# Performance work log

Hardware: AMD Instinct MI355X
Metric: run time of the kernel (lower is better)

The kernel has to match this reference:

```python
import jax, jax.numpy as jnp
import numpy as np
from jax import lax

VOCAB = 4096
HID = 1024
BATCH = 64
SEQ = 256


def setup_inputs() -> dict:
    key = jax.random.key(0)
    ks = jax.random.split(key, 8)
    s = 0.02  # small init to keep gates out of saturation
    return {
        "tokens": jax.random.randint(ks[0], (BATCH, SEQ), 0, VOCAB),
        "W1": jax.random.normal(ks[1], (4, VOCAB + HID, HID), jnp.float32) * s,
        "b1": jax.random.normal(ks[2], (4, HID), jnp.float32) * s,
        "W2": jax.random.normal(ks[3], (4, 2 * HID, HID), jnp.float32) * s,
        "b2": jax.random.normal(ks[4], (4, HID), jnp.float32) * s,
        "Wout": jax.random.normal(ks[5], (HID, VOCAB), jnp.float32) * s,
        "bout": jax.random.normal(ks[6], (VOCAB,), jnp.float32) * s,
    }


def _cell(x, H, C, W, b):
    # x: [B, in], H/C: [B, Hid]; W: [4, in+Hid, Hid] stacked f,i,o,c_tilde
    cat = jnp.concatenate([x, H], axis=1)                 # [B, in+Hid]
    g = jnp.einsum('bd,gdh->gbh', cat, W) + b[:, None, :] # [4, B, Hid]
    f = jax.nn.sigmoid(g[0])
    i = jax.nn.sigmoid(g[1])
    o = jax.nn.sigmoid(g[2])
    c_tilde = jnp.tanh(g[3])
    C = f * C + i * c_tilde
    H = o * jnp.tanh(C)
    return H, C


def reference(tokens, W1, b1, W2, b2, Wout, bout):
    B = tokens.shape[0]
    V = Wout.shape[1]
    Hn = W1.shape[2]
    z = jnp.zeros((B, Hn), dtype=Wout.dtype)
    init = (z, z, z, z)  # (H1, C1, H2, C2), zero initial states

    def step(carry, tok):
        H1, C1, H2, C2 = carry
        x = jax.nn.one_hot(tok, V, dtype=Wout.dtype)  # [B, V]
        H1, C1 = _cell(x, H1, C1, W1, b1)
        H2, C2 = _cell(H1, H2, C2, W2, b2)
        Y = H2 @ Wout + bout                          # [B, V]
        return (H1, C1, H2, C2), Y

    carry, ys = lax.scan(step, init, tokens.T)  # ys: [S, B, V]
    out = ys.reshape(-1, V)                     # torch.cat(outputs, dim=0)
    H1, C1, H2, C2 = carry
    return out, H1, C1, H2, C2
```

## Files before the change

kernel.cpp:

```cpp
#include <hip/hip_runtime.h>
#include <hip/hip_bf16.h>

typedef float f32x4 __attribute__((ext_vector_type(4)));
typedef short bf16x8 __attribute__((ext_vector_type(8)));
typedef unsigned int u32x4 __attribute__((ext_vector_type(4)));

#define MFMA16x32(a,b,c) __builtin_amdgcn_mfma_f32_16x16x32_bf16((a),(b),(c),0,0,0)

__device__ __forceinline__ unsigned short f2bf(float f) {
  unsigned u = __float_as_uint(f);
  u += 0x7fffu + ((u >> 16) & 1u);
  return (unsigned short)(u >> 16);
}

__device__ __forceinline__ void ast16(unsigned short* p, unsigned short v) {
  __hip_atomic_store(p, v, __ATOMIC_RELAXED, __HIP_MEMORY_SCOPE_AGENT);
}

__device__ __forceinline__ u32x4 ld16_bypass(const void* p) {
  u32x4 r;
  asm volatile("global_load_dwordx4 %0, %1, off sc0 sc1" : "=v"(r) : "v"(p) : "memory");
  return r;
}

#define WS_G1BLOB 0ull
#define WS_G3BLOB 8388608ull
#define WS_WOUTT  25165824ull
#define WS_H1RING 33554432ull
#define WS_SYNC   34078720ull
#define WS_H2ALL  34095104ull

#define SLSTRIDE 8

__global__ void k_init(unsigned* __restrict__ p, int n) {
  int i = blockIdx.x * blockDim.x + threadIdx.x;
  for (; i < n; i += gridDim.x * blockDim.x) p[i] = 0u;
}

__global__ void k_pack_g1(const float* __restrict__ W1, unsigned short* __restrict__ blob) {
  int gtid = blockIdx.x * 256 + threadIdx.x;
  int lane = gtid & 63, kk = (gtid >> 6) & 31, w = gtid >> 11;
  int c = lane & 15, q = lane >> 4;
  int g = c >> 2, h = w * 4 + (c & 3);
  bf16x8 s;
#pragma unroll
  for (int j = 0; j < 8; ++j) {
    int k = kk * 32 + q * 8 + j;
    float v = W1[(size_t)g * 5242880u + (size_t)(4096 + k) * 1024u + h];
    ((unsigned short*)&s)[j] = f2bf(v);
  }
  ((bf16x8*)blob)[(size_t)(w * 32 + kk) * 64 + lane] = s;
}

__global__ void k_pack_g3(const float* __restrict__ W2, unsigned short* __restrict__ blob) {
  int gtid = blockIdx.x * 256 + threadIdx.x;
  int lane = gtid & 63, kk = (gtid >> 6) & 63, w = gtid >> 12;
  int c = lane & 15, q = lane >> 4;
  int g = c >> 2, h = w * 4 + (c & 3);
  bf16x8 s;
#pragma unroll
  for (int j = 0; j < 8; ++j) {
    int klocal = (kk & 31) * 32 + q * 8 + j;
    int d = (kk < 32) ? (1024 + klocal) : klocal;
    float v = W2[(size_t)g * 2097152u + (size_t)d * 1024u + h];
    ((unsigned short*)&s)[j] = f2bf(v);
  }
  ((bf16x8*)blob)[(size_t)(w * 64 + kk) * 64 + lane] = s;
}

__global__ void k_pack_woutT(const float* __restrict__ Wout, unsigned short* __restrict__ wT) {
  int gtid = blockIdx.x * 256 + threadIdx.x;
  int k = gtid & 1023, n = gtid >> 10;
  wT[(size_t)n * 1024 + k] = f2bf(Wout[(size_t)k * 4096 + n]);
}

__device__ __forceinline__ void wait_slots(const unsigned* __restrict__ slots,
                                           unsigned epoch, unsigned* __restrict__ poison) {
  if (threadIdx.x < 64) {
    unsigned guard = 0;
    for (;;) {
      unsigned v0 = __hip_atomic_load(&slots[threadIdx.x * SLSTRIDE],
                                      __ATOMIC_RELAXED, __HIP_MEMORY_SCOPE_AGENT);
      unsigned v1 = __hip_atomic_load(&slots[(threadIdx.x + 64) * SLSTRIDE],
                                      __ATOMIC_RELAXED, __HIP_MEMORY_SCOPE_AGENT);
      unsigned v = v0 < v1 ? v0 : v1;
      if (__all((int)(v >= epoch))) break;
      __builtin_amdgcn_s_sleep(1);
      if (((++guard) & 1023u) == 0u) {
        if (guard > (1u << 18) ||
            __hip_atomic_load(poison, __ATOMIC_RELAXED, __HIP_MEMORY_SCOPE_AGENT) != 0u) {
          __hip_atomic_store(poison, 1u, __ATOMIC_RELAXED, __HIP_MEMORY_SCOPE_AGENT);
          break;
        }
      }
    }
  }
  __syncthreads();
}

__device__ __forceinline__ void publish_slot(unsigned* __restrict__ slots,
                                             int myslot, unsigned epoch) {
  asm volatile("s_waitcnt vmcnt(0)" ::: "memory");
  __syncthreads();
  if (threadIdx.x == 0) {
    __hip_atomic_store(&slots[myslot * SLSTRIDE], epoch,
                       __ATOMIC_RELAXED, __HIP_MEMORY_SCOPE_AGENT);
  }
}

__device__ __forceinline__ void stage_H(const unsigned short* __restrict__ Hsrc,
                                        unsigned short* __restrict__ Hs) {
  asm volatile("s_waitcnt vmcnt(0)" ::: "memory");
  const int tid = threadIdx.x;
  const char* base = (const char*)Hsrc;
  const int rowlo = tid >> 7;
  const int x = (tid & 127) * 16;
  u32x4 v[4][8];
#define ISSUE_BATCH(B) \
  _Pragma("unroll") \
  for (int r8 = 0; r8 < 8; ++r8) { \
    int row = ((B) * 8 + r8) * 2 + rowlo; \
    v[B][r8] = ld16_bypass(base + row * 2048 + (x ^ ((row & 7) << 4))); \
  }
#define WRITE_BATCH(B) \
  _Pragma("unroll") \
  for (int r8 = 0; r8 < 8; ++r8) \
    *(u32x4*)((char*)Hs + ((B) * 8 + r8) * 4096 + tid * 16) = v[B][r8];

  ISSUE_BATCH(0)
  ISSUE_BATCH(1)
  asm volatile("s_waitcnt vmcnt(8)" ::: "memory");
  __builtin_amdgcn_sched_barrier(0);
  WRITE_BATCH(0)
  ISSUE_BATCH(2)
  asm volatile("s_waitcnt vmcnt(8)" ::: "memory");
  __builtin_amdgcn_sched_barrier(0);
  WRITE_BATCH(1)
  ISSUE_BATCH(3)
  asm volatile("s_waitcnt vmcnt(8)" ::: "memory");
  __builtin_amdgcn_sched_barrier(0);
  WRITE_BATCH(2)
  asm volatile("s_waitcnt vmcnt(0)" ::: "memory");
  __builtin_amdgcn_sched_barrier(0);
  WRITE_BATCH(3)
#undef ISSUE_BATCH
#undef WRITE_BATCH
}

__device__ __forceinline__ bf16x8 lds_frag(const unsigned short* __restrict__ Hs,
                                           int row, int colb) {
  return *(const bf16x8*)((const char*)Hs + row * 2048 + (colb ^ ((row & 7) << 4)));
}

__global__ __launch_bounds__(256, 1) void k_lstm(
    const int* __restrict__ tokens, const float* __restrict__ W1,
    const float* __restrict__ b1, const float* __restrict__ b2,
    const unsigned short* __restrict__ g1blob, const unsigned short* __restrict__ g3blob,
    unsigned short* __restrict__ h1ring, unsigned short* __restrict__ h2all,
    float* __restrict__ outF, unsigned* __restrict__ syncbase)
{
  __shared__ unsigned short Hs[65536];
  __shared__ float red[2][64][16];

  const int tid = threadIdx.x, lane = tid & 63, widx = tid >> 6, bid = blockIdx.x;
  const int c = lane & 15, q = lane >> 4;
  const bool isG1 = bid < 128;
  const int myslot = isG1 ? bid : bid - 128;
  const int ct = widx >> 1, kh = widx & 1;
  const int w = myslot * 2 + ct;
  const int g = c >> 2;
  const int hcol = w * 4 + (c & 3);
  const int h_ew = w * 4 + (lane & 3);

  unsigned* g1slots = syncbase;
  unsigned* g3slots = syncbase + 1024;
  unsigned* poison  = syncbase + 2048;

  bf16x8 Breg[32];
  {
    const bf16x8* blob1 = (const bf16x8*)g1blob;
    const bf16x8* blob3 = (const bf16x8*)g3blob;
    if (isG1) {
#pragma unroll
      for (int j = 0; j < 16; ++j)
        Breg[j] = blob1[(size_t)(w * 32 + kh * 16 + j) * 64 + lane];
    } else {
#pragma unroll
      for (int j = 0; j < 16; ++j) {
        Breg[j]      = blob3[(size_t)(w * 64 + kh * 16 + j) * 64 + lane];
        Breg[16 + j] = blob3[(size_t)(w * 64 + 32 + kh * 16 + j) * 64 + lane];
      }
    }
  }
  const float biasv = isG1 ? b1[g * 1024 + hcol] : b2[g * 1024 + hcol];

  float Cst[16];
#pragma unroll
  for (int i = 0; i < 16; ++i) Cst[i] = 0.f;

  float gv[16];
  if (isG1 && kh == 0) {
#pragma unroll
    for (int m = 0; m < 4; ++m)
#pragma unroll
      for (int r = 0; r < 4; ++r) {
        int b_ = m * 16 + q * 4 + r;
        int tk = tokens[b_ * 256];
        gv[m * 4 + r] = W1[(size_t)g * 5242880u + (size_t)tk * 1024u + hcol];
      }
  }

  f32x4 acc[4];

  if (isG1) {
#pragma clang loop unroll(disable)
    for (int t = 0; t < 256; ++t) {
      if (t > 0) wait_slots(g1slots, (unsigned)t, poison);

      int tk2[16];
      if (kh == 0) {
        const int tn = (t < 255) ? t + 1 : 255;
#pragma unroll
        for (int m = 0; m < 4; ++m)
#pragma unroll
          for (int r = 0; r < 4; ++r)
            tk2[m * 4 + r] = tokens[(m * 16 + q * 4 + r) * 256 + tn];
      }

#pragma unroll
      for (int m = 0; m < 4; ++m) acc[m] = (f32x4){0.f, 0.f, 0.f, 0.f};
      if (t > 0) {
        stage_H(h1ring + ((t - 1) & 3) * 65536, Hs);
        __syncthreads();
#pragma unroll
        for (int j = 0; j < 16; ++j) {
#pragma unroll
          for (int m = 0; m < 4; ++m) {
            bf16x8 a = lds_frag(Hs, m * 16 + c, (kh * 16 + j) * 64 + q * 16);
            acc[m] = MFMA16x32(a, Breg[j], acc[m]);
          }
        }
      }
      if (t >= 4) wait_slots(g3slots, (unsigned)(t - 3), poison);
      else __syncthreads();

      if (kh == 1) {
#pragma unroll
        for (int m = 0; m < 4; ++m) *(f32x4*)&red[ct][lane][m * 4] = acc[m];
      }
      __syncthreads();
      if (kh == 0) {
#pragma unroll
        for (int m = 0; m < 4; ++m) acc[m] += *(const f32x4*)&red[ct][lane][m * 4];
#pragma unroll
        for (int m = 0; m < 4; ++m) {
#pragma unroll
          for (int r = 0; r < 4; ++r) {
            float v = acc[m][r] + gv[m * 4 + r] + biasv;
            const int sb = (lane & 48) | (lane & 3);
            float vf = __shfl(v, sb, 64);
            float vi = __shfl(v, sb | 4, 64);
            float vo = __shfl(v, sb | 8, 64);
            float vc = __shfl(v, sb | 12, 64);
            float fg = 1.f / (1.f + __expf(-vf));
            float ig = 1.f / (1.f + __expf(-vi));
            float og = 1.f / (1.f + __expf(-vo));
            float e2 = __expf(2.f * vc);
            float ct_ = (e2 - 1.f) / (e2 + 1.f);
            float Cn = fg * Cst[m * 4 + r] + ig * ct_;
            Cst[m * 4 + r] = Cn;
            float e2c = __expf(2.f * Cn);
            float Hn = og * (e2c - 1.f) / (e2c + 1.f);
            if ((lane & 12) == 0) {
              int row = m * 16 + q * 4 + r;
              ast16(&h1ring[(t & 3) * 65536 + row * 1024 + h_ew], f2bf(Hn));
              if (t == 255) {
                outF[row * 1024 + h_ew] = Hn;
                outF[65536 + row * 1024 + h_ew] = Cn;
              }
            }
          }
        }
      }
      publish_slot(g1slots, myslot, (unsigned)(t + 1));

      if (kh == 0) {
#pragma unroll
        for (int i = 0; i < 16; ++i)
          gv[i] = W1[(size_t)g * 5242880u + (size_t)tk2[i] * 1024u + hcol];
      }
    }
  } else {
#pragma clang loop unroll(disable)
    for (int t = 0; t < 256; ++t) {
      wait_slots(g1slots, (unsigned)(t + 1), poison);
#pragma unroll
      for (int m = 0; m < 4; ++m)
        acc[m] = (kh == 0) ? (f32x4){biasv, biasv, biasv, biasv}
                           : (f32x4){0.f, 0.f, 0.f, 0.f};
      stage_H(h1ring + (t & 3) * 65536, Hs);
      __syncthreads();
#pragma unroll
      for (int j = 0; j < 16; ++j) {
#pragma unroll
        for (int m = 0; m < 4; ++m) {
          bf16x8 a = lds_frag(Hs, m * 16 + c, (kh * 16 + j) * 64 + q * 16);
          acc[m] = MFMA16x32(a, Breg[16 + j], acc[m]);
        }
      }

      if (t > 0) {
        wait_slots(g3slots, (unsigned)t, poison);
        stage_H(h2all + (size_t)(t - 1) * 65536, Hs);
        __syncthreads();
#pragma unroll
        for (int j = 0; j < 16; ++j) {
#pragma unroll
          for (int m = 0; m < 4; ++m) {
            bf16x8 a = lds_frag(Hs, m * 16 + c, (kh * 16 + j) * 64 + q * 16);
            acc[m] = MFMA16x32(a, Breg[j], acc[m]);
          }
        }
      }

      if (kh == 1) {
#pragma unroll
        for (int m = 0; m < 4; ++m) *(f32x4*)&red[ct][lane][m * 4] = acc[m];
      }
      __syncthreads();
      if (kh == 0) {
#pragma unroll
        for (int m = 0; m < 4; ++m) acc[m] += *(const f32x4*)&red[ct][lane][m * 4];
#pragma unroll
        for (int m = 0; m < 4; ++m) {
#pragma unroll
          for (int r = 0; r < 4; ++r) {
            float v = acc[m][r];
            const int sb = (lane & 48) | (lane & 3);
            float vf = __shfl(v, sb, 64);
            float vi = __shfl(v, sb | 4, 64);
            float vo = __shfl(v, sb | 8, 64);
            float vc = __shfl(v, sb | 12, 64);
            float fg = 1.f / (1.f + __expf(-vf));
            float ig = 1.f / (1.f + __expf(-vi));
            float og = 1.f / (1.f + __expf(-vo));
            float e2 = __expf(2.f * vc);
            float ct_ = (e2 - 1.f) / (e2 + 1.f);
            float Cn = fg * Cst[m * 4 + r] + ig * ct_;
            Cst[m * 4 + r] = Cn;
            float e2c = __expf(2.f * Cn);
            float Hn = og * (e2c - 1.f) / (e2c + 1.f);
            if ((lane & 12) == 0) {
              int row = m * 16 + q * 4 + r;
              ast16(&h2all[((size_t)t * 64 + row) * 1024 + h_ew], f2bf(Hn));
              if (t == 255) {
                outF[131072 + row * 1024 + h_ew] = Hn;
                outF[196608 + row * 1024 + h_ew] = Cn;
              }
            }
          }
        }
      }
      publish_slot(g3slots, myslot, (unsigned)(t + 1));
    }
  }
}

__global__ __launch_bounds__(256, 2) void k_gemm_out(
    const unsigned short* __restrict__ A, const unsigned short* __restrict__ Bt,
    const float* __restrict__ bout, float* __restrict__ C)
{
  __shared__ unsigned short As[128 * 32];
  __shared__ unsigned short Bs[128 * 32];
  const int tid = threadIdx.x, lane = tid & 63, wv = tid >> 6;
  const int c = lane & 15, q = lane >> 4;
  const int bn = blockIdx.x & 31, bm = blockIdx.x >> 5;
  const int wm = wv >> 1, wn = wv & 1;

  f32x4 acc[4][4];
#pragma unroll
  for (int m = 0; m < 4; ++m)
#pragma unroll
    for (int n = 0; n < 4; ++n) acc[m][n] = (f32x4){0.f, 0.f, 0.f, 0.f};

  const unsigned short* Abase = A + (size_t)(bm * 128) * 1024;
  const unsigned short* Bbase = Bt + (size_t)(bn * 128) * 1024;

  for (int kt = 0; kt < 32; ++kt) {
    if (kt) __syncthreads();
#pragma unroll
    for (int ch = 0; ch < 2; ++ch) {
      int o = ch * 4096 + tid * 16;
      int row = o >> 6;
      int ks = (o & 63) >> 1;
      *(bf16x8*)&As[o >> 1] = *(const bf16x8*)(Abase + (size_t)row * 1024 + kt * 32 + ks);
      *(bf16x8*)&Bs[o >> 1] = *(const bf16x8*)(Bbase + (size_t)row * 1024 + kt * 32 + ks);
    }
    __syncthreads();
    bf16x8 af[4], bfr[4];
#pragma unroll
    for (int m = 0; m < 4; ++m) af[m] = *(const bf16x8*)&As[(wm * 64 + m * 16 + c) * 32 + q * 8];
#pragma unroll
    for (int n = 0; n < 4; ++n) bfr[n] = *(const bf16x8*)&Bs[(wn * 64 + n * 16 + c) * 32 + q * 8];
#pragma unroll
    for (int m = 0; m < 4; ++m)
#pragma unroll
      for (int n = 0; n < 4; ++n) acc[m][n] = MFMA16x32(af[m], bfr[n], acc[m][n]);
  }

#pragma unroll
  for (int n = 0; n < 4; ++n) {
    int col = bn * 128 + wn * 64 + n * 16 + c;
    float bo = bout[col];
#pragma unroll
    for (int m = 0; m < 4; ++m) {
      int row0 = bm * 128 + wm * 64 + m * 16 + q * 4;
#pragma unroll
      for (int r = 0; r < 4; ++r)
        C[(size_t)(row0 + r) * 4096 + col] = acc[m][n][r] + bo;
    }
  }
}

extern "C" void kernel_launch(void* const* d_in, const int* in_sizes, int n_in,
                              void* d_out, int out_size, void* d_ws, size_t ws_size,
                              hipStream_t stream) {
  const int* tokens = (const int*)d_in[0];
  const float* W1 = (const float*)d_in[1];
  const float* b1 = (const float*)d_in[2];
  const float* W2 = (const float*)d_in[3];
  const float* b2 = (const float*)d_in[4];
  const float* Wout = (const float*)d_in[5];
  const float* bout = (const float*)d_in[6];

  char* ws = (char*)d_ws;
  unsigned short* g1blob = (unsigned short*)(ws + WS_G1BLOB);
  unsigned short* g3blob = (unsigned short*)(ws + WS_G3BLOB);
  unsigned short* woutT  = (unsigned short*)(ws + WS_WOUTT);
  unsigned short* h1ring = (unsigned short*)(ws + WS_H1RING);
  unsigned*       syncb  = (unsigned*)(ws + WS_SYNC);
  unsigned short* h2all  = (unsigned short*)(ws + WS_H2ALL);

  float* outY = (float*)d_out;
  float* outF = outY + 67108864;

  hipLaunchKernelGGL(k_init, dim3(16), dim3(256), 0, stream, syncb, 4096);
  hipLaunchKernelGGL(k_pack_g1, dim3(2048), dim3(256), 0, stream, W1, g1blob);
  hipLaunchKernelGGL(k_pack_g3, dim3(4096), dim3(256), 0, stream, W2, g3blob);
  hipLaunchKernelGGL(k_pack_woutT, dim3(16384), dim3(256), 0, stream, Wout, woutT);

  hipLaunchKernelGGL(k_lstm, dim3(256), dim3(256), 0, stream,
                     tokens, W1, b1, b2, g1blob, g3blob, h1ring, h2all, outF, syncb);

  hipLaunchKernelGGL(k_gemm_out, dim3(4096), dim3(256), 0, stream, h2all, woutT, bout, outY);
}
```

Before: 2.768 ms.

## Load MFMA A-fragments directly from global memory instead of staging H through LDS

Result: slower. 5.213 ms (+88.4%).

```diff
diff --git a/kernel.cpp b/kernel.cpp
--- a/kernel.cpp
+++ b/kernel.cpp
@@ -17,8 +17,8 @@
   __hip_atomic_store(p, v, __ATOMIC_RELAXED, __HIP_MEMORY_SCOPE_AGENT);
 }
 
-__device__ __forceinline__ u32x4 ld16_bypass(const void* p) {
-  u32x4 r;
+__device__ __forceinline__ bf16x8 ld16f(const void* p) {
+  bf16x8 r;
   asm volatile("global_load_dwordx4 %0, %1, off sc0 sc1" : "=v"(r) : "v"(p) : "memory");
   return r;
 }
@@ -108,48 +108,34 @@
   }
 }
 
-__device__ __forceinline__ void stage_H(const unsigned short* __restrict__ Hsrc,
-                                        unsigned short* __restrict__ Hs) {
+__device__ __forceinline__ void phase_direct(const char* __restrict__ Hbase,
+                                             int kh, int c, int q,
+                                             const bf16x8* __restrict__ Bw,
+                                             f32x4 (&acc)[4]) {
   asm volatile("s_waitcnt vmcnt(0)" ::: "memory");
-  const int tid = threadIdx.x;
-  const char* base = (const char*)Hsrc;
-  const int rowlo = tid >> 7;
-  const int x = (tid & 127) * 16;
-  u32x4 v[4][8];
-#define ISSUE_BATCH(B) \
-  _Pragma("unroll") \
-  for (int r8 = 0; r8 < 8; ++r8) { \
-    int row = ((B) * 8 + r8) * 2 + rowlo; \
-    v[B][r8] = ld16_bypass(base + row * 2048 + (x ^ ((row & 7) << 4))); \
-  }
-#define WRITE_BATCH(B) \
-  _Pragma("unroll") \
-  for (int r8 = 0; r8 < 8; ++r8) \
-    *(u32x4*)((char*)Hs + ((B) * 8 + r8) * 4096 + tid * 16) = v[B][r8];
-
-  ISSUE_BATCH(0)
-  ISSUE_BATCH(1)
-  asm volatile("s_waitcnt vmcnt(8)" ::: "memory");
-  __builtin_amdgcn_sched_barrier(0);
-  WRITE_BATCH(0)
-  ISSUE_BATCH(2)
-  asm volatile("s_waitcnt vmcnt(8)" ::: "memory");
-  __builtin_amdgcn_sched_barrier(0);
-  WRITE_BATCH(1)
-  ISSUE_BATCH(3)
-  asm volatile("s_waitcnt vmcnt(8)" ::: "memory");
-  __builtin_amdgcn_sched_barrier(0);
-  WRITE_BATCH(2)
-  asm volatile("s_waitcnt vmcnt(0)" ::: "memory");
-  __builtin_amdgcn_sched_barrier(0);
-  WRITE_BATCH(3)
-#undef ISSUE_BATCH
-#undef WRITE_BATCH
-}
-
-__device__ __forceinline__ bf16x8 lds_frag(const unsigned short* __restrict__ Hs,
-                                           int row, int colb) {
-  return *(const bf16x8*)((const char*)Hs + row * 2048 + (colb ^ ((row & 7) << 4)));
+  const char* base = Hbase + c * 2048 + kh * 1024 + q * 16;
+  bf16x8 v[2][8];
+#define ISSUE(BUF, M, JB) \
+  _Pragma("unroll") for (int i = 0; i < 8; ++i) \
+    v[BUF][i] = ld16f(base + (M) * 32768 + ((JB) * 8 + i) * 64);
+#define MM(BUF, M, JB) \
+  _Pragma("unroll") for (int i = 0; i < 8; ++i) \
+    acc[M] = MFMA16x32(v[BUF][i], Bw[(JB) * 8 + i], acc[M]);
+#define W8 asm volatile("s_waitcnt vmcnt(8)" ::: "memory"); __builtin_amdgcn_sched_barrier(0);
+#define W0 asm volatile("s_waitcnt vmcnt(0)" ::: "memory"); __builtin_amdgcn_sched_barrier(0);
+  ISSUE(0, 0, 0) ISSUE(1, 0, 1)
+  W8 MM(0, 0, 0) ISSUE(0, 1, 0)
+  W8 MM(1, 0, 1) ISSUE(1, 1, 1)
+  W8 MM(0, 1, 0) ISSUE(0, 2, 0)
+  W8 MM(1, 1, 1) ISSUE(1, 2, 1)
+  W8 MM(0, 2, 0) ISSUE(0, 3, 0)
+  W8 MM(1, 2, 1) ISSUE(1, 3, 1)
+  W8 MM(0, 3, 0)
+  W0 MM(1, 3, 1)
+#undef ISSUE
+#undef MM
+#undef W8
+#undef W0
 }
 
 __global__ __launch_bounds__(256, 1) void k_lstm(
@@ -159,8 +145,7 @@
     unsigned short* __restrict__ h1ring, unsigned short* __restrict__ h2all,
     float* __restrict__ outF, unsigned* __restrict__ syncbase)
 {
-  __shared__ unsigned short Hs[65536];
-  __shared__ float red[2][64][16];
+  __shared__ float red[2][16][64];
 
   const int tid = threadIdx.x, lane = tid & 63, widx = tid >> 6, bid = blockIdx.x;
   const int c = lane & 15, q = lane >> 4;
@@ -229,34 +214,24 @@
 
 #pragma unroll
       for (int m = 0; m < 4; ++m) acc[m] = (f32x4){0.f, 0.f, 0.f, 0.f};
-      if (t > 0) {
-        stage_H(h1ring + ((t - 1) & 3) * 65536, Hs);
-        __syncthreads();
-#pragma unroll
-        for (int j = 0; j < 16; ++j) {
-#pragma unroll
-          for (int m = 0; m < 4; ++m) {
-            bf16x8 a = lds_frag(Hs, m * 16 + c, (kh * 16 + j) * 64 + q * 16);
-            acc[m] = MFMA16x32(a, Breg[j], acc[m]);
-          }
-        }
-      }
+      if (t > 0)
+        phase_direct((const char*)(h1ring + ((t - 1) & 3) * 65536), kh, c, q, &Breg[0], acc);
+
       if (t >= 4) wait_slots(g3slots, (unsigned)(t - 3), poison);
-      else __syncthreads();
 
       if (kh == 1) {
 #pragma unroll
-        for (int m = 0; m < 4; ++m) *(f32x4*)&red[ct][lane][m * 4] = acc[m];
+        for (int m = 0; m < 4; ++m)
+#pragma unroll
+          for (int r = 0; r < 4; ++r) red[ct][m * 4 + r][lane] = acc[m][r];
       }
       __syncthreads();
       if (kh == 0) {
 #pragma unroll
-        for (int m = 0; m < 4; ++m) acc[m] += *(const f32x4*)&red[ct][lane][m * 4];
-#pragma unroll
         for (int m = 0; m < 4; ++m) {
 #pragma unroll
           for (int r = 0; r < 4; ++r) {
-            float v = acc[m][r] + gv[m * 4 + r] + biasv;
+            float v = acc[m][r] + red[ct][m * 4 + r][lane] + gv[m * 4 + r] + biasv;
             const int sb = (lane & 48) | (lane & 3);
             float vf = __shfl(v, sb, 64);
             float vi = __shfl(v, sb | 4, 64);
@@ -298,44 +273,26 @@
       for (int m = 0; m < 4; ++m)
         acc[m] = (kh == 0) ? (f32x4){biasv, biasv, biasv, biasv}
                            : (f32x4){0.f, 0.f, 0.f, 0.f};
-      stage_H(h1ring + (t & 3) * 65536, Hs);
-      __syncthreads();
-#pragma unroll
-      for (int j = 0; j < 16; ++j) {
-#pragma unroll
-        for (int m = 0; m < 4; ++m) {
-          bf16x8 a = lds_frag(Hs, m * 16 + c, (kh * 16 + j) * 64 + q * 16);
-          acc[m] = MFMA16x32(a, Breg[16 + j], acc[m]);
-        }
-      }
+      phase_direct((const char*)(h1ring + (t & 3) * 65536), kh, c, q, &Breg[16], acc);
 
       if (t > 0) {
         wait_slots(g3slots, (unsigned)t, poison);
-        stage_H(h2all + (size_t)(t - 1) * 65536, Hs);
-        __syncthreads();
-#pragma unroll
-        for (int j = 0; j < 16; ++j) {
-#pragma unroll
-          for (int m = 0; m < 4; ++m) {
-            bf16x8 a = lds_frag(Hs, m * 16 + c, (kh * 16 + j) * 64 + q * 16);
-            acc[m] = MFMA16x32(a, Breg[j], acc[m]);
-          }
-        }
+        phase_direct((const char*)(h2all + (size_t)(t - 1) * 65536), kh, c, q, &Breg[0], acc);
       }
 
       if (kh == 1) {
 #pragma unroll
-        for (int m = 0; m < 4; ++m) *(f32x4*)&red[ct][lane][m * 4] = acc[m];
+        for (int m = 0; m < 4; ++m)
+#pragma unroll
+          for (int r = 0; r < 4; ++r) red[ct][m * 4 + r][lane] = acc[m][r];
       }
       __syncthreads();
       if (kh == 0) {
 #pragma unroll
-        for (int m = 0; m < 4; ++m) acc[m] += *(const f32x4*)&red[ct][lane][m * 4];
-#pragma unroll
         for (int m = 0; m < 4; ++m) {
 #pragma unroll
           for (int r = 0; r < 4; ++r) {
-            float v = acc[m][r];
+            float v = acc[m][r] + red[ct][m * 4 + r][lane];
             const int sb = (lane & 48) | (lane & 3);
             float vf = __shfl(v, sb, 64);
             float vi = __shfl(v, sb | 4, 64);
```
